# Optimization experiments

Hardware: AMD Instinct MI355X
Metric: run time of the kernel (lower is better)

## Reference

```python
import jax, jax.numpy as jnp
import numpy as np

SEG_LENS = (2048, 4096, 8192)
DIL_RATES = (1, 2, 4)
NUM_HEADS = 12
HEAD_DIM = 64
LN_EPS = 1e-5


def _dilated_attention(q, k, v):
    # q,k,v: [b, n, h, d]; heads partitioned across (segment, dilation) groups
    b, n, h, d = q.shape
    G = len(SEG_LENS)
    hg = h // G
    scale = d ** -0.5
    out = jnp.zeros_like(q)
    for i, (s, r) in enumerate(zip(SEG_LENS, DIL_RATES)):
        hmin = i * hg
        m = n // s                      # number of segments
        idx = jnp.arange(i % r, s, r)   # dilated positions within a segment, len = s // r
        def seg(t):
            # [b, n, hg, d] -> [b, m, s//r, hg, d]
            return t[:, :, hmin:hmin + hg, :].reshape(b, m, s, hg, d)[:, :, idx]
        qs, ks, vs = seg(q), seg(k), seg(v)
        scores = jnp.einsum('bmshd,bmthd->bmhst', qs, ks) * scale  # [b,m,hg,s/r,s/r]
        attn = jax.nn.softmax(scores, axis=-1)
        o = jnp.einsum('bmhst,bmthd->bmshd', attn, vs)              # [b,m,s/r,hg,d]
        pos = (jnp.arange(m)[:, None] * s + idx[None, :]).reshape(-1)
        out = out.at[:, pos, hmin:hmin + hg, :].set(o.reshape(b, -1, hg, d))
    return out


def setup_inputs() -> dict:
    key = jax.random.key(0)
    ks = jax.random.split(key, 4)
    E = NUM_HEADS * HEAD_DIM
    b, n = 1, 8192
    x = jax.random.normal(ks[0], (b, n, E), dtype=jnp.float32)
    w_qkv = jax.random.normal(ks[1], (3 * E, E), dtype=jnp.float32) * (E ** -0.5)
    b_qkv = jnp.zeros((3 * E,), dtype=jnp.float32)
    w_out = jax.random.normal(ks[2], (E, E), dtype=jnp.float32) * (E ** -0.5)
    b_out = jnp.zeros((E,), dtype=jnp.float32)
    ln_gamma = jnp.ones((E,), dtype=jnp.float32)
    ln_beta = jnp.zeros((E,), dtype=jnp.float32)
    return {'x': x, 'w_qkv': w_qkv, 'b_qkv': b_qkv, 'w_out': w_out,
            'b_out': b_out, 'ln_gamma': ln_gamma, 'ln_beta': ln_beta}


def reference(x, w_qkv, b_qkv, w_out, b_out, ln_gamma, ln_beta):
    b, n, E = x.shape
    qkv = x @ w_qkv.T + b_qkv
    q, k, v = jnp.split(qkv, 3, axis=-1)
    shp = (b, n, NUM_HEADS, HEAD_DIM)
    o = _dilated_attention(q.reshape(shp), k.reshape(shp), v.reshape(shp)).reshape(b, n, E)
    # MAGNETO: LayerNorm on attention output before out projection
    mu = jnp.mean(o, axis=-1, keepdims=True)
    var = jnp.mean(jnp.square(o - mu), axis=-1, keepdims=True)
    on = (o - mu) / jnp.sqrt(var + LN_EPS) * ln_gamma + ln_beta
    return on @ w_out.T + b_out
```

## Files before the change

kernel.cpp:

```cpp
#include <hip/hip_runtime.h>
#include <hip/hip_bf16.h>
#include <cstdint>
#include <cstddef>


typedef __attribute__((ext_vector_type(8))) short short8;
typedef __attribute__((ext_vector_type(4))) short short4_;
typedef __attribute__((ext_vector_type(4))) float float4_;
typedef __attribute__((ext_vector_type(16))) float floatx16;
typedef __attribute__((ext_vector_type(4))) int int4_;

#if __has_builtin(__builtin_amdgcn_exp2f)
#define EXP2(x) __builtin_amdgcn_exp2f(x)
#else
#define EXP2(x) exp2f(x)
#endif

__device__ __forceinline__ float bf2f(short s) {
    unsigned int u = ((unsigned int)(unsigned short)s) << 16;
    float f;
    __builtin_memcpy(&f, &u, 4);
    return f;
}
__device__ __forceinline__ short f2bf(float f) {
    unsigned int u;
    __builtin_memcpy(&u, &f, 4);
    u += 0x7fffu + ((u >> 16) & 1u);
    return (short)(u >> 16);
}
__device__ __forceinline__ short8 f8_to_bf8(const float* __restrict__ p) {
    float4_ a = *(const float4_*)(p);
    float4_ b = *(const float4_*)(p + 4);
    short8 r;
    r[0] = f2bf(a[0]); r[1] = f2bf(a[1]); r[2] = f2bf(a[2]); r[3] = f2bf(a[3]);
    r[4] = f2bf(b[0]); r[5] = f2bf(b[1]); r[6] = f2bf(b[2]); r[7] = f2bf(b[3]);
    return r;
}
__device__ __forceinline__ void gll16(const short* g, short* l) {
    __builtin_amdgcn_global_load_lds(
        (const __attribute__((address_space(1))) unsigned int*)g,
        (__attribute__((address_space(3))) unsigned int*)l, 16, 0, 0);
}
__device__ __forceinline__ int cvtpk(float lo, float hi) {
    int r;
    asm("v_cvt_pk_bf16_f32 %0, %1, %2" : "=v"(r) : "v"(lo), "v"(hi));
    return r;
}

#define LDT 72

__global__ __launch_bounds__(256) void cvt3(
    const float* __restrict__ a, int na, const float* __restrict__ b, int nb,
    const float* __restrict__ c, int nc,
    short* __restrict__ oa, short* __restrict__ ob, short* __restrict__ oc)
{
    int i = (blockIdx.x * 256 + threadIdx.x) * 8;
    if (i < na) {
        *(short8*)&oa[i] = f8_to_bf8(a + i);
    } else if (i < na + nb) {
        int j = i - na;
        *(short8*)&ob[j] = f8_to_bf8(b + j);
    } else {
        int j = i - na - nb;
        if (j < nc) *(short8*)&oc[j] = f8_to_bf8(c + j);
    }
}

__global__ __launch_bounds__(256) void gemm_qkv(
    const short* __restrict__ A,
    const short* __restrict__ B,
    const float* __restrict__ bias,
    short* __restrict__ C)
{
    __shared__ short As[128 * 64];
    __shared__ short Bs[64 * 64];

    const int bx = blockIdx.x;
    const int L  = (bx & 7) * 168 + (bx >> 3);
    int g, t, rate, off0;
    if (L < 768)       { g = 0; t = L;        rate = 1; off0 = 0; }
    else if (L < 1152) { g = 1; t = L - 768;  rate = 2; off0 = 1; }
    else               { g = 2; t = L - 1152; rate = 4; off0 = 2; }
    const int nx = t % 12, my = t / 12;
    const int ncol0 = (nx >> 2) * 768 + g * 256 + (nx & 3) * 64;
    const int m0 = my * 128;

    const int tid  = threadIdx.x;
    const int wave = tid >> 6, lane = tid & 63;
    const int quad = lane >> 4, l16 = lane & 15;
    const int lrow   = lane >> 3;
    const int lchunk = (lane & 7) ^ lrow;

    const short* Abase = A + (size_t)(off0 + (m0 + wave * 32 + lrow) * rate) * 768
                           + lchunk * 8;
    const short* Bbase = B + (size_t)(ncol0 + wave * 16 + lrow) * 768 + lchunk * 8;
    short* AsW = &As[(wave * 32) * 64];
    short* BsW = &Bs[(wave * 16) * 64];
    const size_t arowstep = (size_t)8 * rate * 768;

    float4_ acc[2][4] = {};

    for (int k0 = 0; k0 < 768; k0 += 64) {
        __syncthreads();
        #pragma unroll
        for (int i = 0; i < 4; i++)
            gll16(Abase + (size_t)i * arowstep + k0, AsW + (i * 8) * 64);
        #pragma unroll
        for (int i = 0; i < 2; i++)
            gll16(Bbase + (size_t)(i * 8) * 768 + k0, BsW + (i * 8) * 64);
        __syncthreads();
        #pragma unroll
        for (int ks = 0; ks < 2; ks++) {
            const int ca = ((ks * 4 + quad) ^ (l16 & 7)) * 8;
            short8 af[2], bf[4];
            #pragma unroll
            for (int mt = 0; mt < 2; mt++)
                af[mt] = *(const short8*)&As[(wave * 32 + mt * 16 + l16) * 64 + ca];
            #pragma unroll
            for (int nt = 0; nt < 4; nt++)
                bf[nt] = *(const short8*)&Bs[(nt * 16 + l16) * 64 + ca];
            #pragma unroll
            for (int mt = 0; mt < 2; mt++)
                #pragma unroll
                for (int nt = 0; nt < 4; nt++)
                    acc[mt][nt] = __builtin_amdgcn_mfma_f32_16x16x32_bf16(
                        af[mt], bf[nt], acc[mt][nt], 0, 0, 0);
        }
    }

    #pragma unroll
    for (int nt = 0; nt < 4; nt++) {
        const int gcol = ncol0 + nt * 16 + l16;
        const float bv = bias[gcol];
        #pragma unroll
        for (int mt = 0; mt < 2; mt++) {
            #pragma unroll
            for (int r = 0; r < 4; r++) {
                const int rl = m0 + wave * 32 + mt * 16 + quad * 4 + r;
                const size_t grow = (size_t)off0 + (size_t)rl * rate;
                C[grow * 2304 + gcol] = f2bf(acc[mt][nt][r] + bv);
            }
        }
    }
}

__global__ __launch_bounds__(256) void gemm_out(
    const short* __restrict__ A,
    const short* __restrict__ B,
    const float* __restrict__ bias,
    float* __restrict__ C)
{
    __shared__ short As[128 * 64];
    __shared__ short Bs[64 * 64];

    const int bx = blockIdx.x;
    const int L  = (bx & 7) * 96 + (bx >> 3);
    const int nx = L % 12, my = L / 12;
    const int n0 = nx * 64, m0 = my * 128;

    const int tid  = threadIdx.x;
    const int wave = tid >> 6, lane = tid & 63;
    const int quad = lane >> 4, l16 = lane & 15;
    const int lrow   = lane >> 3;
    const int lchunk = (lane & 7) ^ lrow;

    const short* Abase = A + (size_t)(m0 + wave * 32 + lrow) * 2304 + lchunk * 8;
    const short* Bbase = B + (size_t)(n0 + wave * 16 + lrow) * 768 + lchunk * 8;
    short* AsW = &As[(wave * 32) * 64];
    short* BsW = &Bs[(wave * 16) * 64];

    float4_ acc[2][4] = {};

    for (int k0 = 0; k0 < 768; k0 += 64) {
        __syncthreads();
        #pragma unroll
        for (int i = 0; i < 4; i++)
            gll16(Abase + (size_t)(i * 8) * 2304 + k0, AsW + (i * 8) * 64);
        #pragma unroll
        for (int i = 0; i < 2; i++)
            gll16(Bbase + (size_t)(i * 8) * 768 + k0, BsW + (i * 8) * 64);
        __syncthreads();
        #pragma unroll
        for (int ks = 0; ks < 2; ks++) {
            const int ca = ((ks * 4 + quad) ^ (l16 & 7)) * 8;
            short8 af[2], bf[4];
            #pragma unroll
            for (int mt = 0; mt < 2; mt++)
                af[mt] = *(const short8*)&As[(wave * 32 + mt * 16 + l16) * 64 + ca];
            #pragma unroll
            for (int nt = 0; nt < 4; nt++)
                bf[nt] = *(const short8*)&Bs[(nt * 16 + l16) * 64 + ca];
            #pragma unroll
            for (int mt = 0; mt < 2; mt++)
                #pragma unroll
                for (int nt = 0; nt < 4; nt++)
                    acc[mt][nt] = __builtin_amdgcn_mfma_f32_16x16x32_bf16(
                        af[mt], bf[nt], acc[mt][nt], 0, 0, 0);
        }
    }

    #pragma unroll
    for (int nt = 0; nt < 4; nt++) {
        const int col = n0 + nt * 16 + l16;
        const float bv = bias[col];
        #pragma unroll
        for (int mt = 0; mt < 2; mt++) {
            #pragma unroll
            for (int r = 0; r < 4; r++) {
                const int row = m0 + wave * 32 + mt * 16 + quad * 4 + r;
                C[(size_t)row * 768 + col] = acc[mt][nt][r] + bv;
            }
        }
    }
}

__global__ __launch_bounds__(256, 4) void dilated_attn(
    const short* __restrict__ qkv, short* __restrict__ obuf1,
    short* __restrict__ obuf2, float* __restrict__ lbuf)
{
    __shared__ short Ks[2 * 64 * 64];
    __shared__ short Vt[2 * 64 * LDT];

    const int bx = blockIdx.x;
    const int L  = (bx & 7) * 112 + (bx >> 3);
    const int qt   = L & 15;
    const int half = (L >> 4) & 1;
    const int sh   = L >> 5;

    int g, seg, s, rate, off0;
    if (sh < 16)      { g = 0; seg = sh >> 2;        s = 2048; rate = 1; off0 = 0; }
    else if (sh < 24) { g = 1; seg = (sh - 16) >> 2; s = 4096; rate = 2; off0 = 1; }
    else              { g = 2; seg = 0;              s = 8192; rate = 4; off0 = 2; }
    const int head = g * 4 + (sh & 3);

    const int tid  = threadIdx.x;
    const int wave = tid >> 6, lane = tid & 63;
    const int h = lane >> 5, l32 = lane & 31;
    const int srow = tid >> 2, scol = (tid & 3) * 16;

    const size_t bpos = (size_t)seg * s + off0
                      + (size_t)(qt * 128 + wave * 32) * rate;
    short8 aq[4];
    {
        const short* qsrc = qkv + (bpos + (size_t)l32 * rate) * 2304
                                + head * 64 + h * 8;
        #pragma unroll
        for (int kt = 0; kt < 4; kt++) {
            short8 q = *(const short8*)(qsrc + kt * 16);
            #pragma unroll
            for (int e = 0; e < 8; e++) q[e] = f2bf(bf2f(q[e]) * 0.1803368801111244f);
            aq[kt] = q;
        }
    }

    const int krow0  = wave * 8 + (lane >> 3);
    const int kchunk = (lane & 7) ^ (lane >> 3);
    const size_t kstep = (size_t)64 * rate * 2304;
    const size_t kq0 = (size_t)seg * s + off0 + (size_t)(half * 1024) * rate;
    const short* kg0 = qkv + (kq0 + (size_t)krow0 * rate) * 2304
                           + 768 + head * 64 + kchunk * 8;
    const short* kg1 = kg0 + (size_t)32 * rate * 2304;
    const short* vgp = qkv + (kq0 + (size_t)srow * rate) * 2304
                           + 1536 + head * 64 + scol;
    const int kofsA = (wave * 8) * 64;
    const int kofsB = kofsA + 32 * 64;
    const int vswz  = scol;

    gll16(kg0, &Ks[kofsA]);
    gll16(kg1, &Ks[kofsB]);
    kg0 += kstep; kg1 += kstep;
    short8 va0 = *(const short8*)(vgp);
    short8 va1 = *(const short8*)(vgp + 8);
    vgp += kstep;
    #pragma unroll
    for (int e = 0; e < 8; e++) Vt[(scol + e) * LDT + (srow ^ vswz)] = va0[e];
    #pragma unroll
    for (int e = 0; e < 8; e++) Vt[(scol + 8 + e) * LDT + (srow ^ vswz)] = va1[e];
    va0 = *(const short8*)(vgp);
    va1 = *(const short8*)(vgp + 8);
    vgp += kstep;

    float lsum = 0.f;
    floatx16 oacc[2] = {};

    auto compute = [&](const short* kb, const short* vb) {
        floatx16 sacc[2] = {};
        __builtin_amdgcn_s_setprio(1);
        #pragma unroll
        for (int kt = 0; kt < 4; kt++) {
            #pragma unroll
            for (int t = 0; t < 2; t++) {
                short8 ak = *(const short8*)&kb[(t * 32 + l32) * 64
                                                + (((kt * 2 + h) ^ (l32 & 7)) * 8)];
                sacc[t] = __builtin_amdgcn_mfma_f32_32x32x16_bf16(
                    ak, aq[kt], sacc[t], 0, 0, 0);
            }
        }
        __builtin_amdgcn_s_setprio(0);

        #pragma unroll
        for (int e = 0; e < 16; e++) {
            float pa_ = EXP2(sacc[0][e]);
            float pb_ = EXP2(sacc[1][e]);
            sacc[0][e] = pa_; sacc[1][e] = pb_;
            lsum += pa_ + pb_;
        }

        short8 pa[4];
        #pragma unroll
        for (int kt = 0; kt < 4; kt++) {
            const int t = kt >> 1, b = (kt & 1) * 8;
            int A1 = cvtpk(sacc[t][b + 0], sacc[t][b + 1]);
            int A2 = cvtpk(sacc[t][b + 2], sacc[t][b + 3]);
            int B1 = cvtpk(sacc[t][b + 4], sacc[t][b + 5]);
            int B2 = cvtpk(sacc[t][b + 6], sacc[t][b + 7]);
            asm volatile("v_permlane32_swap_b32 %0, %1" : "+v"(A1), "+v"(B1));
            asm volatile("v_permlane32_swap_b32 %0, %1" : "+v"(A2), "+v"(B2));
            int4_ w; w[0] = A1; w[1] = A2; w[2] = B1; w[3] = B2;
            __builtin_memcpy(&pa[kt], &w, 16);
        }

        __builtin_amdgcn_s_setprio(1);
        #pragma unroll
        for (int kt = 0; kt < 4; kt++) {
            #pragma unroll
            for (int dt = 0; dt < 2; dt++) {
                const int d = dt * 32 + l32;
                short8 bv = *(const short8*)&vb[d * LDT
                                                + ((kt ^ ((d >> 4) & 3)) * 16 + h * 8)];
                oacc[dt] = __builtin_amdgcn_mfma_f32_32x32x16_bf16(
                    pa[kt], bv, oacc[dt], 0, 0, 0);
            }
        }
        __builtin_amdgcn_s_setprio(0);
    };

    for (int j = 0; j < 15; j++) {
        asm volatile("s_waitcnt vmcnt(2)" ::: "memory");
        asm volatile("s_waitcnt lgkmcnt(0)" ::: "memory");
        __builtin_amdgcn_s_barrier();

        const int nb = (j + 1) & 1;
        gll16(kg0, &Ks[nb * 4096 + kofsA]);
        gll16(kg1, &Ks[nb * 4096 + kofsB]);
        kg0 += kstep; kg1 += kstep;
        asm volatile("s_waitcnt vmcnt(2)" ::: "memory");
        short* vt = &Vt[nb * 64 * LDT];
        #pragma unroll
        for (int e = 0; e < 8; e++) vt[(scol + e) * LDT + (srow ^ vswz)] = va0[e];
        #pragma unroll
        for (int e = 0; e < 8; e++) vt[(scol + 8 + e) * LDT + (srow ^ vswz)] = va1[e];
        if (j < 14) {
            va0 = *(const short8*)(vgp);
            va1 = *(const short8*)(vgp + 8);
            vgp += kstep;
        }
        compute(&Ks[(j & 1) * 4096], &Vt[(j & 1) * 64 * LDT]);
    }
    asm volatile("s_waitcnt vmcnt(0)" ::: "memory");
    asm volatile("s_waitcnt lgkmcnt(0)" ::: "memory");
    __builtin_amdgcn_s_barrier();
    compute(&Ks[4096], &Vt[64 * LDT]);

    {
        short* obase = half ? obuf2 : obuf1;
        float* lb = lbuf + (size_t)half * 8192 * 12;
        float lt = lsum + __shfl_xor(lsum, 32, 64);
        #pragma unroll
        for (int m = 0; m < 4; m++) {
            #pragma unroll
            for (int r = 0; r < 4; r++) {
                const int ql = 4 * h + r + 8 * m;
                short* od = obase + (bpos + (size_t)ql * rate) * 768 + head * 64;
                od[l32]      = f2bf(oacc[0][m * 4 + r]);
                od[32 + l32] = f2bf(oacc[1][m * 4 + r]);
            }
        }
        if (lane < 32)
            lb[(bpos + (size_t)l32 * rate) * 12 + head] = lt;
    }
}

__global__ __launch_bounds__(256) void ln_inplace(
    short* __restrict__ qkv, const short* __restrict__ obuf1,
    const short* __restrict__ obuf2, const float* __restrict__ lbuf,
    const float* __restrict__ gamma, const float* __restrict__ beta)
{
    const int row  = blockIdx.x * 4 + (threadIdx.x >> 6);
    const int lane = threadIdx.x & 63;
    const short* s1 = obuf1 + (size_t)row * 768;
    const short* s2 = obuf2 + (size_t)row * 768;
    short* dst = qkv + (size_t)row * 2304;

    const int h1 = lane >> 3;
    const int h2 = 8 + (lane >> 4);
    const bool cov1 = (h1 < 4) || ((row & 1) == 1);
    const bool cov2 = ((row & 3) == 2);
    const float li1 = cov1
        ? 1.0f / (lbuf[row * 12 + h1] + lbuf[8192 * 12 + row * 12 + h1]) : 0.0f;
    const float li2 = cov2
        ? 1.0f / (lbuf[row * 12 + h2] + lbuf[8192 * 12 + row * 12 + h2]) : 0.0f;

    short8  a  = *(const short8*)&s1[lane * 8];
    short4_ b  = *(const short4_*)&s1[512 + lane * 4];
    short8  a2 = *(const short8*)&s2[lane * 8];
    short4_ b2 = *(const short4_*)&s2[512 + lane * 4];
    float v[12];
    #pragma unroll
    for (int e = 0; e < 8; e++)
        v[e] = cov1 ? (bf2f(a[e]) + bf2f(a2[e])) * li1 : 0.0f;
    #pragma unroll
    for (int e = 0; e < 4; e++)
        v[8 + e] = cov2 ? (bf2f(b[e]) + bf2f(b2[e])) * li2 : 0.0f;

    float sum = 0.f, sq = 0.f;
    #pragma unroll
    for (int e = 0; e < 12; e++) { sum += v[e]; sq += v[e] * v[e]; }
    #pragma unroll
    for (int off = 1; off < 64; off <<= 1) {
        sum += __shfl_xor(sum, off, 64);
        sq  += __shfl_xor(sq,  off, 64);
    }
    float mean = sum * (1.0f / 768.0f);
    float var  = sq * (1.0f / 768.0f) - mean * mean;
    float rstd = rsqrtf(var + 1e-5f);

    short8 o8; short4_ o4;
    #pragma unroll
    for (int e = 0; e < 8; e++)
        o8[e] = f2bf((v[e] - mean) * rstd * gamma[lane * 8 + e] + beta[lane * 8 + e]);
    #pragma unroll
    for (int e = 0; e < 4; e++)
        o4[e] = f2bf((v[8 + e] - mean) * rstd * gamma[512 + lane * 4 + e] + beta[512 + lane * 4 + e]);

    *(short8*)&dst[lane * 8] = o8;
    *(short4_*)&dst[512 + lane * 4] = o4;
}

extern "C" void kernel_launch(void* const* d_in, const int* in_sizes, int n_in,
                              void* d_out, int out_size, void* d_ws, size_t ws_size,
                              hipStream_t stream) {
    const float* x     = (const float*)d_in[0];
    const float* w_qkv = (const float*)d_in[1];
    const float* b_qkv = (const float*)d_in[2];
    const float* w_out = (const float*)d_in[3];
    const float* b_out = (const float*)d_in[4];
    const float* gamma = (const float*)d_in[5];
    const float* beta  = (const float*)d_in[6];
    float* out = (float*)d_out;

    const int NX = 8192 * 768, NW1 = 2304 * 768, NW2 = 768 * 768;
    char* ws = (char*)d_ws;
    short* qkv   = (short*)(ws);
    short* xb    = (short*)(ws + (size_t)8192 * 2304 * 2);
    short* wqkvb = xb + NX;
    short* woutb = wqkvb + NW1;
    float* lbuf  = (float*)(woutb + NW2);
    short* obuf2 = (short*)(lbuf + 2 * 8192 * 12);
    short* obuf1 = xb;

    cvt3<<<dim3((NX + NW1 + NW2) / (256 * 8)), 256, 0, stream>>>(
        x, NX, w_qkv, NW1, w_out, NW2, xb, wqkvb, woutb);

    gemm_qkv<<<dim3(1344), 256, 0, stream>>>(xb, wqkvb, b_qkv, qkv);

    dilated_attn<<<dim3(28 * 2 * 16), 256, 0, stream>>>(qkv, obuf1, obuf2, lbuf);

    ln_inplace<<<dim3(8192 / 4), 256, 0, stream>>>(
        qkv, obuf1, obuf2, lbuf, gamma, beta);

    gemm_out<<<dim3(768), 256, 0, stream>>>(qkv, woutb, b_out, out);
}
```

Before: 183.4 us.

## Process 64 query rows per wave in dilated attention to reuse K/V tiles

Each wave now handles two 32-row query groups instead of one, so every K and V tile loaded into shared memory feeds twice as many MFMAs. The grid shrinks from 896 to 448 blocks, the block-index remap is adjusted to match, and launch bounds drop from 4 to 2 blocks per CU to leave room for the doubled accumulators. This cuts global and LDS traffic per query. The cost is fewer blocks in flight and more register pressure, with 448 blocks on 256 CUs giving an uneven tail.

```diff
diff --git a/kernel.cpp b/kernel.cpp
--- a/kernel.cpp
+++ b/kernel.cpp
@@ -214,7 +214,7 @@
     }
 }
 
-__global__ __launch_bounds__(256, 4) void dilated_attn(
+__global__ __launch_bounds__(256, 2) void dilated_attn(
     const short* __restrict__ qkv, short* __restrict__ obuf1,
     short* __restrict__ obuf2, float* __restrict__ lbuf)
 {
@@ -222,10 +222,10 @@
     __shared__ short Vt[2 * 64 * LDT];
 
     const int bx = blockIdx.x;
-    const int L  = (bx & 7) * 112 + (bx >> 3);
-    const int qt   = L & 15;
-    const int half = (L >> 4) & 1;
-    const int sh   = L >> 5;
+    const int L  = (bx & 7) * 56 + (bx >> 3);
+    const int qt   = L & 7;
+    const int half = (L >> 3) & 1;
+    const int sh   = L >> 4;
 
     int g, seg, s, rate, off0;
     if (sh < 16)      { g = 0; seg = sh >> 2;        s = 2048; rate = 1; off0 = 0; }
@@ -239,17 +239,18 @@
     const int srow = tid >> 2, scol = (tid & 3) * 16;
 
     const size_t bpos = (size_t)seg * s + off0
-                      + (size_t)(qt * 128 + wave * 32) * rate;
-    short8 aq[4];
-    {
-        const short* qsrc = qkv + (bpos + (size_t)l32 * rate) * 2304
+                      + (size_t)(qt * 256 + wave * 64) * rate;
+    short8 aq[2][4];
+    #pragma unroll
+    for (int rg = 0; rg < 2; rg++) {
+        const short* qsrc = qkv + (bpos + (size_t)(rg * 32 + l32) * rate) * 2304
                                 + head * 64 + h * 8;
         #pragma unroll
         for (int kt = 0; kt < 4; kt++) {
             short8 q = *(const short8*)(qsrc + kt * 16);
             #pragma unroll
             for (int e = 0; e < 8; e++) q[e] = f2bf(bf2f(q[e]) * 0.1803368801111244f);
-            aq[kt] = q;
+            aq[rg][kt] = q;
         }
     }
 
@@ -280,11 +281,11 @@
     va1 = *(const short8*)(vgp + 8);
     vgp += kstep;
 
-    float lsum = 0.f;
-    floatx16 oacc[2] = {};
+    float lsum[2] = {};
+    floatx16 oacc[2][2] = {};
 
     auto compute = [&](const short* kb, const short* vb) {
-        floatx16 sacc[2] = {};
+        floatx16 sacc[2][2] = {};
         __builtin_amdgcn_s_setprio(1);
         #pragma unroll
         for (int kt = 0; kt < 4; kt++) {
@@ -292,32 +293,36 @@
             for (int t = 0; t < 2; t++) {
                 short8 ak = *(const short8*)&kb[(t * 32 + l32) * 64
                                                 + (((kt * 2 + h) ^ (l32 & 7)) * 8)];
-                sacc[t] = __builtin_amdgcn_mfma_f32_32x32x16_bf16(
-                    ak, aq[kt], sacc[t], 0, 0, 0);
+                #pragma unroll
+                for (int rg = 0; rg < 2; rg++)
+                    sacc[rg][t] = __builtin_amdgcn_mfma_f32_32x32x16_bf16(
+                        ak, aq[rg][kt], sacc[rg][t], 0, 0, 0);
             }
         }
         __builtin_amdgcn_s_setprio(0);
 
-        #pragma unroll
-        for (int e = 0; e < 16; e++) {
-            float pa_ = EXP2(sacc[0][e]);
-            float pb_ = EXP2(sacc[1][e]);
-            sacc[0][e] = pa_; sacc[1][e] = pb_;
-            lsum += pa_ + pb_;
-        }
-
-        short8 pa[4];
-        #pragma unroll
-        for (int kt = 0; kt < 4; kt++) {
-            const int t = kt >> 1, b = (kt & 1) * 8;
-            int A1 = cvtpk(sacc[t][b + 0], sacc[t][b + 1]);
-            int A2 = cvtpk(sacc[t][b + 2], sacc[t][b + 3]);
-            int B1 = cvtpk(sacc[t][b + 4], sacc[t][b + 5]);
-            int B2 = cvtpk(sacc[t][b + 6], sacc[t][b + 7]);
-            asm volatile("v_permlane32_swap_b32 %0, %1" : "+v"(A1), "+v"(B1));
-            asm volatile("v_permlane32_swap_b32 %0, %1" : "+v"(A2), "+v"(B2));
-            int4_ w; w[0] = A1; w[1] = A2; w[2] = B1; w[3] = B2;
-            __builtin_memcpy(&pa[kt], &w, 16);
+        short8 pa[2][4];
+        #pragma unroll
+        for (int rg = 0; rg < 2; rg++) {
+            #pragma unroll
+            for (int e = 0; e < 16; e++) {
+                float pa_ = EXP2(sacc[rg][0][e]);
+                float pb_ = EXP2(sacc[rg][1][e]);
+                sacc[rg][0][e] = pa_; sacc[rg][1][e] = pb_;
+                lsum[rg] += pa_ + pb_;
+            }
+            #pragma unroll
+            for (int kt = 0; kt < 4; kt++) {
+                const int t = kt >> 1, b = (kt & 1) * 8;
+                int A1 = cvtpk(sacc[rg][t][b + 0], sacc[rg][t][b + 1]);
+                int A2 = cvtpk(sacc[rg][t][b + 2], sacc[rg][t][b + 3]);
+                int B1 = cvtpk(sacc[rg][t][b + 4], sacc[rg][t][b + 5]);
+                int B2 = cvtpk(sacc[rg][t][b + 6], sacc[rg][t][b + 7]);
+                asm volatile("v_permlane32_swap_b32 %0, %1" : "+v"(A1), "+v"(B1));
+                asm volatile("v_permlane32_swap_b32 %0, %1" : "+v"(A2), "+v"(B2));
+                int4_ w; w[0] = A1; w[1] = A2; w[2] = B1; w[3] = B2;
+                __builtin_memcpy(&pa[rg][kt], &w, 16);
+            }
         }
 
         __builtin_amdgcn_s_setprio(1);
@@ -328,8 +333,10 @@
                 const int d = dt * 32 + l32;
                 short8 bv = *(const short8*)&vb[d * LDT
                                                 + ((kt ^ ((d >> 4) & 3)) * 16 + h * 8)];
-                oacc[dt] = __builtin_amdgcn_mfma_f32_32x32x16_bf16(
-                    pa[kt], bv, oacc[dt], 0, 0, 0);
+                #pragma unroll
+                for (int rg = 0; rg < 2; rg++)
+                    oacc[rg][dt] = __builtin_amdgcn_mfma_f32_32x32x16_bf16(
+                        pa[rg][kt], bv, oacc[rg][dt], 0, 0, 0);
             }
         }
         __builtin_amdgcn_s_setprio(0);
@@ -365,19 +372,22 @@
     {
         short* obase = half ? obuf2 : obuf1;
         float* lb = lbuf + (size_t)half * 8192 * 12;
-        float lt = lsum + __shfl_xor(lsum, 32, 64);
-        #pragma unroll
-        for (int m = 0; m < 4; m++) {
-            #pragma unroll
-            for (int r = 0; r < 4; r++) {
-                const int ql = 4 * h + r + 8 * m;
-                short* od = obase + (bpos + (size_t)ql * rate) * 768 + head * 64;
-                od[l32]      = f2bf(oacc[0][m * 4 + r]);
-                od[32 + l32] = f2bf(oacc[1][m * 4 + r]);
-            }
-        }
-        if (lane < 32)
-            lb[(bpos + (size_t)l32 * rate) * 12 + head] = lt;
+        #pragma unroll
+        for (int rg = 0; rg < 2; rg++) {
+            float lt = lsum[rg] + __shfl_xor(lsum[rg], 32, 64);
+            #pragma unroll
+            for (int m = 0; m < 4; m++) {
+                #pragma unroll
+                for (int r = 0; r < 4; r++) {
+                    const int ql = rg * 32 + 4 * h + r + 8 * m;
+                    short* od = obase + (bpos + (size_t)ql * rate) * 768 + head * 64;
+                    od[l32]      = f2bf(oacc[rg][0][m * 4 + r]);
+                    od[32 + l32] = f2bf(oacc[rg][1][m * 4 + r]);
+                }
+            }
+            if (lane < 32)
+                lb[(bpos + (size_t)(rg * 32 + l32) * rate) * 12 + head] = lt;
+        }
     }
 }
 
@@ -464,7 +474,7 @@
 
     gemm_qkv<<<dim3(1344), 256, 0, stream>>>(xb, wqkvb, b_qkv, qkv);
 
-    dilated_attn<<<dim3(28 * 2 * 16), 256, 0, stream>>>(qkv, obuf1, obuf2, lbuf);
+    dilated_attn<<<dim3(448), 256, 0, stream>>>(qkv, obuf1, obuf2, lbuf);
 
     ln_inplace<<<dim3(8192 / 4), 256, 0, stream>>>(
         qkv, obuf1, obuf2, lbuf, gamma, beta);
```

Measured after the change: 183.1 us. Within noise of the previous version (-0.2%).
